# Kernel optimization log

Measured on AMD Instinct MI355X. Metric: run time of the kernel, lower is better.

Reference implementation:

```python
import jax, jax.numpy as jnp
import numpy as np

LN_EPS = 1e-5
NORM_EPS = 1e-6
ALPHA = 0.5

def _normalize_xyz_with_pc(pc, xyz):
    # center by point-cloud centroid, scale by max radius (per batch)
    c = pc.mean(axis=1, keepdims=True)                      # [B,1,3]
    scale = jnp.linalg.norm(pc - c, axis=-1).max(axis=1)    # [B]
    return (xyz - c) / (scale[:, None, None] + NORM_EPS)

def setup_inputs() -> dict:
    key = jax.random.key(0)
    ks = jax.random.split(key, 9)
    B, N, Ns, K, Dv, Dc = 4, 20000, 1024, 8192, 768, 256
    return {
        "point_cloud": jax.random.normal(ks[0], (B, N, 3), jnp.float32),
        "seed_xyz": jax.random.normal(ks[1], (B, Ns, 3), jnp.float32),
        "pts": jax.random.normal(ks[2], (B, K, 3), jnp.float32),
        "feat": jax.random.normal(ks[3], (B, Dv, K), jnp.float32),
        "f_graspnet": jax.random.normal(ks[4], (B, Dc, Ns), jnp.float32),
        "W_proj": jax.random.normal(ks[5], (Dc, Dv), jnp.float32) * 0.02,
        "b_proj": jnp.zeros((Dc,), jnp.float32),
        "W_a1": jax.random.normal(ks[6], (Dc, Dc), jnp.float32) * 0.05,
        "b_a1": jnp.zeros((Dc,), jnp.float32),
        "W_a2": jax.random.normal(ks[7], (Dc, Dc), jnp.float32) * 0.05,
        "b_a2": jnp.zeros((Dc,), jnp.float32),
    }

def reference(point_cloud, seed_xyz, pts, feat, f_graspnet,
              W_proj, b_proj, W_a1, b_a1, W_a2, b_a2):
    seed_n = _normalize_xyz_with_pc(point_cloud, seed_xyz)   # [B,Ns,3]
    pts_n = _normalize_xyz_with_pc(point_cloud, pts)         # [B,K,3]
    # squared pairwise distances [B,Ns,K] (argmin equivalent to cdist argmin)
    d2 = ((seed_n ** 2).sum(-1)[:, :, None]
          - 2.0 * jnp.einsum('bnd,bkd->bnk', seed_n, pts_n)
          + (pts_n ** 2).sum(-1)[:, None, :])
    idx = jnp.argmin(d2, axis=-1)                            # [B,Ns]
    vggt_raw = jnp.take_along_axis(feat, idx[:, None, :], axis=2)  # [B,768,Ns]
    # 1x1 conv projector 768->256
    x = jnp.einsum('oc,bcn->bon', W_proj, vggt_raw) + b_proj[None, :, None]
    # LayerNorm over channel dim, no affine
    mu = x.mean(axis=1, keepdims=True)
    var = ((x - mu) ** 2).mean(axis=1, keepdims=True)
    x_ln = (x - mu) / jnp.sqrt(var + LN_EPS)
    # adapter: conv-relu-conv (all 1x1)
    h = jax.nn.relu(jnp.einsum('oc,bcn->bon', W_a1, x_ln) + b_a1[None, :, None])
    f_adapt = jnp.einsum('oc,bcn->bon', W_a2, h) + b_a2[None, :, None]
    return (1.0 - ALPHA) * f_graspnet + ALPHA * f_adapt
```

## Files before the change

kernel.cpp:

```cpp
#include <hip/hip_runtime.h>
#include <hip/hip_bf16.h>
#include <math.h>

#define LN_EPS 1e-5f

constexpr int BB  = 4;
constexpr int NS  = 1024;
constexpr int KP  = 8192;
constexpr int DV  = 768;
constexpr int DC  = 256;

using bf16x8 = __attribute__((ext_vector_type(8))) short;
using f32x4  = __attribute__((ext_vector_type(4))) float;

static __device__ __forceinline__ unsigned short f2bf(float v) {
    __hip_bfloat16 h = __float2bfloat16(v);
    return *reinterpret_cast<unsigned short*>(&h);
}

__global__ __launch_bounds__(256) void argmin_prep_kernel(
    const float* __restrict__ seed_xyz, const float* __restrict__ pts,
    int* __restrict__ out_idx,
    const float* __restrict__ Wp, const float* __restrict__ W1,
    const float* __restrict__ W2,
    unsigned short* __restrict__ Wpb, unsigned short* __restrict__ W1b,
    unsigned short* __restrict__ W2b)
{
    const int t = threadIdx.x;
    if (blockIdx.x >= 512) {
        int e  = (blockIdx.x - 512) * 256 + t;
        int e4 = e << 2;
        const float* src; unsigned short* dst; int off;
        if (e4 < DC * DV)              { src = Wp; dst = Wpb; off = e4; }
        else if (e4 < DC * (DV + DC))  { src = W1; dst = W1b; off = e4 - DC * DV; }
        else                           { src = W2; dst = W2b; off = e4 - DC * (DV + DC); }
        float4 v = *(const float4*)(src + off);
        ushort4 o;
        o.x = f2bf(v.x); o.y = f2bf(v.y); o.z = f2bf(v.z); o.w = f2bf(v.w);
        *(ushort4*)(dst + off) = o;
        return;
    }

    __shared__ float shX[1024], shY[1024], shZ[1024];
    __shared__ double rb[4][8];
    __shared__ int    ri[4][8];

    const int bid  = blockIdx.x;
    const int b    = bid >> 7;
    const int tile = bid & 127;

    double n2sx[8], n2sy[8], n2sz[8];
    {
        const float* sp = seed_xyz + ((size_t)b * NS + tile * 8) * 3;
        #pragma unroll
        for (int ss = 0; ss < 8; ++ss) {
            n2sx[ss] = -2.0 * (double)sp[ss * 3 + 0];
            n2sy[ss] = -2.0 * (double)sp[ss * 3 + 1];
            n2sz[ss] = -2.0 * (double)sp[ss * 3 + 2];
        }
    }

    const float* pb = pts + (size_t)b * KP * 3;
    double best[8];
    int    bidx[8];
    #pragma unroll
    for (int ss = 0; ss < 8; ++ss) { best[ss] = 1e300; bidx[ss] = 0; }

    for (int kt = 0; kt < KP; kt += 1024) {
        #pragma unroll
        for (int q = 0; q < 4; ++q) {
            int i = t + q * 256;
            const float* pp = pb + (size_t)(kt + i) * 3;
            shX[i] = pp[0]; shY[i] = pp[1]; shZ[i] = pp[2];
        }
        __syncthreads();
        #pragma unroll 2
        for (int q = 0; q < 4; ++q) {
            int kl = t + (q << 8);
            double px = (double)shX[kl];
            double py = (double)shY[kl];
            double pz = (double)shZ[kl];
            double h  = fma(px, px, fma(py, py, pz * pz));
            #pragma unroll
            for (int ss = 0; ss < 8; ++ss) {
                double acc = fma(n2sx[ss], px, h);
                acc = fma(n2sy[ss], py, acc);
                acc = fma(n2sz[ss], pz, acc);
                if (acc < best[ss]) { best[ss] = acc; bidx[ss] = kt + kl; }
            }
        }
        __syncthreads();
    }

    #pragma unroll
    for (int o = 1; o < 64; o <<= 1) {
        #pragma unroll
        for (int ss = 0; ss < 8; ++ss) {
            double ob = __shfl_xor(best[ss], o);
            int    oi = __shfl_xor(bidx[ss], o);
            if (ob < best[ss] || (ob == best[ss] && oi < bidx[ss])) {
                best[ss] = ob; bidx[ss] = oi;
            }
        }
    }
    const int w = t >> 6, l = t & 63;
    if (l == 0) {
        #pragma unroll
        for (int ss = 0; ss < 8; ++ss) { rb[w][ss] = best[ss]; ri[w][ss] = bidx[ss]; }
    }
    __syncthreads();
    if (t < 8) {
        double bb = rb[0][t]; int bi = ri[0][t];
        #pragma unroll
        for (int ww = 1; ww < 4; ++ww) {
            double ob = rb[ww][t]; int oi = ri[ww][t];
            if (ob < bb || (ob == bb && oi < bi)) { bb = ob; bi = oi; }
        }
        out_idx[b * NS + tile * 8 + t] = bi;
    }
}

__global__ __launch_bounds__(512, 4) void proj_kernel(
    const float* __restrict__ feat, const int* __restrict__ idx,
    const unsigned short* __restrict__ Wpb, float* __restrict__ Xg)
{
    __shared__ unsigned short LDSB[64 * 40];
    __shared__ int ent_s[1024];
    __shared__ int ent_k[1024];
    __shared__ int nent;

    const int bid = blockIdx.x;
    const int b   = bid >> 7;
    const int kt  = bid & 127;
    const int k0  = kt * 64;
    const int t   = threadIdx.x;
    const int w   = t >> 6;
    const int l   = t & 63;
    const int col = l & 15;
    const int kq  = l >> 4;

    if (t == 0) nent = 0;
    __syncthreads();
    {
        int ka = idx[b * NS + t];
        int kb = idx[b * NS + 512 + t];
        if (ka >= k0 && ka < k0 + 64) { int p = atomicAdd(&nent, 1); ent_s[p] = t;       ent_k[p] = ka; }
        if (kb >= k0 && kb < k0 + 64) { int p = atomicAdd(&nent, 1); ent_s[p] = 512 + t; ent_k[p] = kb; }
    }

    const int cc = t >> 4;
    const int k4 = t & 15;
    const float* fbase = feat + ((size_t)b * DV + cc) * KP + k0 + k4 * 4;

    f32x4 acc0[4], acc1[4];
    #pragma unroll
    for (int kg = 0; kg < 4; ++kg) {
        acc0[kg] = (f32x4){0.f, 0.f, 0.f, 0.f};
        acc1[kg] = (f32x4){0.f, 0.f, 0.f, 0.f};
    }

    f32x4 r = *(const f32x4*)(fbase);
    for (int s = 0; s < 24; ++s) {
        if (s) __syncthreads();
        {
            const int kr0 = k4 * 4;
            const int cb  = cc >> 3;
            const int cl  = cc & 7;
            #pragma unroll
            for (int i = 0; i < 4; ++i) {
                int krow = kr0 + i;
                int qv   = ((krow >> 2) ^ (krow >> 4)) & 3;
                LDSB[krow * 40 + ((cb ^ qv) << 3) + cl] = f2bf(r[i]);
            }
        }
        if (s + 1 < 24)
            r = *(const f32x4*)(fbase + (size_t)(s + 1) * 32 * KP);
        __syncthreads();
        const unsigned short* A0 = Wpb + (size_t)(w * 32 + col) * DV + s * 32 + kq * 8;
        bf16x8 a0 = *(const bf16x8*)A0;
        bf16x8 a1 = *(const bf16x8*)(A0 + (size_t)16 * DV);
        #pragma unroll
        for (int kg = 0; kg < 4; ++kg) {
            int krow = kg * 16 + col;
            int qv   = ((krow >> 2) ^ (krow >> 4)) & 3;
            bf16x8 bf = *(const bf16x8*)&LDSB[krow * 40 + ((kq ^ qv) << 3)];
            acc0[kg] = __builtin_amdgcn_mfma_f32_16x16x32_bf16(a0, bf, acc0[kg], 0, 0, 0);
            acc1[kg] = __builtin_amdgcn_mfma_f32_16x16x32_bf16(a1, bf, acc1[kg], 0, 0, 0);
        }
    }
    __syncthreads();

    const int ne = nent;
    for (int e = 0; e < ne; ++e) {
        int sd = ent_s[e];
        int kk = ent_k[e] - k0;
        if (col == (kk & 15)) {
            int j = kk >> 4;
            float* dst = Xg + ((size_t)(b * NS + sd)) * DC + w * 32 + kq * 4;
            #pragma unroll
            for (int jj = 0; jj < 4; ++jj) if (jj == j) {
                *(f32x4*)dst        = acc0[jj];
                *(f32x4*)(dst + 16) = acc1[jj];
            }
        }
    }
}

__global__ __launch_bounds__(512) void mega_kernel(
    const float* __restrict__ Xg,
    const float* __restrict__ fg,
    const float* __restrict__ bp,
    const unsigned short* __restrict__ W1b, const float* __restrict__ b1,
    const unsigned short* __restrict__ W2b, const float* __restrict__ b2,
    float* __restrict__ out)
{
    __shared__ alignas(16) unsigned short XT[16][264];
    __shared__ alignas(16) unsigned short HT[16][264];
    __shared__ float LNs[8][16];
    __shared__ float LNq[8][16];

    const int bid  = blockIdx.x;
    const int b    = bid >> 6;
    const int tile = bid & 63;
    const int n0   = tile * 16;
    const int t    = threadIdx.x;
    const int w    = t >> 6;
    const int l    = t & 63;
    const int col  = l & 15;
    const int kq   = l >> 4;

    const float* fgb = fg + (size_t)b * DC * NS;
    float fgv[8];
    #pragma unroll
    for (int r = 0; r < 4; ++r) {
        int ch0 = w * 32 + kq * 4 + r;
        fgv[r]     = fgb[(size_t)ch0 * NS + n0 + col];
        fgv[4 + r] = fgb[(size_t)(ch0 + 16) * NS + n0 + col];
    }

    const float* xr = Xg + ((size_t)(b * NS + n0 + col)) * DC + w * 32 + kq * 4;
    f32x4 x0 = *(const f32x4*)xr;
    f32x4 x1 = *(const f32x4*)(xr + 16);

    float vals[8];
    float s = 0.f, q = 0.f;
    #pragma unroll
    for (int r = 0; r < 4; ++r) {
        int ch0 = w * 32 + kq * 4 + r;
        float v0 = x0[r] + bp[ch0];
        float v1 = x1[r] + bp[ch0 + 16];
        vals[r]     = v0;
        vals[4 + r] = v1;
        s += v0 + v1;
        q += v0 * v0 + v1 * v1;
    }
    s += __shfl_xor(s, 16); s += __shfl_xor(s, 32);
    q += __shfl_xor(q, 16); q += __shfl_xor(q, 32);
    if (l < 16) { LNs[w][l] = s; LNq[w][l] = q; }
    __syncthreads();
    float S = 0.f, Q = 0.f;
    #pragma unroll
    for (int ww = 0; ww < 8; ++ww) { S += LNs[ww][col]; Q += LNq[ww][col]; }
    float mu   = S * (1.0f / DC);
    float rstd = rsqrtf(Q * (1.0f / DC) - mu * mu + LN_EPS);
    {
        ushort4 p0, p1;
        p0.x = f2bf((vals[0] - mu) * rstd);
        p0.y = f2bf((vals[1] - mu) * rstd);
        p0.z = f2bf((vals[2] - mu) * rstd);
        p0.w = f2bf((vals[3] - mu) * rstd);
        p1.x = f2bf((vals[4] - mu) * rstd);
        p1.y = f2bf((vals[5] - mu) * rstd);
        p1.z = f2bf((vals[6] - mu) * rstd);
        p1.w = f2bf((vals[7] - mu) * rstd);
        *(ushort4*)&XT[col][w * 32 + kq * 4]      = p0;
        *(ushort4*)&XT[col][w * 32 + 16 + kq * 4] = p1;
    }
    __syncthreads();

    f32x4 acc0 = {0.f, 0.f, 0.f, 0.f};
    f32x4 acc1 = {0.f, 0.f, 0.f, 0.f};
    {
        const unsigned short* A0 = W1b + (size_t)(w * 32 + col) * DC;
        const unsigned short* A1 = W1b + (size_t)(w * 32 + 16 + col) * DC;
        #pragma unroll
        for (int ks = 0; ks < 8; ++ks) {
            int kb = ks * 32 + kq * 8;
            bf16x8 bf = *(const bf16x8*)&XT[col][kb];
            bf16x8 a0 = *(const bf16x8*)&A0[kb];
            bf16x8 a1 = *(const bf16x8*)&A1[kb];
            acc0 = __builtin_amdgcn_mfma_f32_16x16x32_bf16(a0, bf, acc0, 0, 0, 0);
            acc1 = __builtin_amdgcn_mfma_f32_16x16x32_bf16(a1, bf, acc1, 0, 0, 0);
        }
    }
    {
        ushort4 p0, p1;
        int ch0 = w * 32 + kq * 4;
        p0.x = f2bf(fmaxf(acc0[0] + b1[ch0 + 0], 0.f));
        p0.y = f2bf(fmaxf(acc0[1] + b1[ch0 + 1], 0.f));
        p0.z = f2bf(fmaxf(acc0[2] + b1[ch0 + 2], 0.f));
        p0.w = f2bf(fmaxf(acc0[3] + b1[ch0 + 3], 0.f));
        p1.x = f2bf(fmaxf(acc1[0] + b1[ch0 + 16], 0.f));
        p1.y = f2bf(fmaxf(acc1[1] + b1[ch0 + 17], 0.f));
        p1.z = f2bf(fmaxf(acc1[2] + b1[ch0 + 18], 0.f));
        p1.w = f2bf(fmaxf(acc1[3] + b1[ch0 + 19], 0.f));
        *(ushort4*)&HT[col][ch0]      = p0;
        *(ushort4*)&HT[col][ch0 + 16] = p1;
    }
    __syncthreads();

    acc0 = (f32x4){0.f, 0.f, 0.f, 0.f};
    acc1 = (f32x4){0.f, 0.f, 0.f, 0.f};
    {
        const unsigned short* A0 = W2b + (size_t)(w * 32 + col) * DC;
        const unsigned short* A1 = W2b + (size_t)(w * 32 + 16 + col) * DC;
        #pragma unroll
        for (int ks = 0; ks < 8; ++ks) {
            int kb = ks * 32 + kq * 8;
            bf16x8 bf = *(const bf16x8*)&HT[col][kb];
            bf16x8 a0 = *(const bf16x8*)&A0[kb];
            bf16x8 a1 = *(const bf16x8*)&A1[kb];
            acc0 = __builtin_amdgcn_mfma_f32_16x16x32_bf16(a0, bf, acc0, 0, 0, 0);
            acc1 = __builtin_amdgcn_mfma_f32_16x16x32_bf16(a1, bf, acc1, 0, 0, 0);
        }
    }
    {
        float* ob = out + (size_t)b * DC * NS;
        #pragma unroll
        for (int r = 0; r < 4; ++r) {
            int ch0 = w * 32 + kq * 4 + r;
            int ch1 = ch0 + 16;
            size_t o0 = (size_t)ch0 * NS + n0 + col;
            size_t o1 = (size_t)ch1 * NS + n0 + col;
            ob[o0] = 0.5f * fgv[r]     + 0.5f * (acc0[r] + b2[ch0]);
            ob[o1] = 0.5f * fgv[4 + r] + 0.5f * (acc1[r] + b2[ch1]);
        }
    }
}

extern "C" void kernel_launch(void* const* d_in, const int* in_sizes, int n_in,
                              void* d_out, int out_size, void* d_ws, size_t ws_size,
                              hipStream_t stream)
{
    (void)in_sizes; (void)n_in; (void)out_size; (void)ws_size;
    const float* seed_xyz = (const float*)d_in[1];
    const float* pts      = (const float*)d_in[2];
    const float* feat     = (const float*)d_in[3];
    const float* fgn      = (const float*)d_in[4];
    const float* Wp       = (const float*)d_in[5];
    const float* bp       = (const float*)d_in[6];
    const float* W1       = (const float*)d_in[7];
    const float* b1       = (const float*)d_in[8];
    const float* W2       = (const float*)d_in[9];
    const float* b2       = (const float*)d_in[10];
    float* out = (float*)d_out;

    char* ws = (char*)d_ws;
    int*            idx = (int*)ws;
    unsigned short* Wpb = (unsigned short*)(ws + 16384);
    unsigned short* W1b = (unsigned short*)(ws + 409600);
    unsigned short* W2b = (unsigned short*)(ws + 540672);
    float*          Xg  = (float*)(ws + 671744);

    argmin_prep_kernel<<<dim3(832), dim3(256), 0, stream>>>(
        seed_xyz, pts, idx, Wp, W1, W2, Wpb, W1b, W2b);
    proj_kernel<<<dim3(512), dim3(512), 0, stream>>>(feat, idx, Wpb, Xg);
    mega_kernel<<<dim3(BB * (NS / 16)), dim3(512), 0, stream>>>(
        Xg, fgn, bp, W1b, b1, W2b, b2, out);
}
```

Before: 66.76 us.

## Fuse projection with LN/adapter kernel, double-buffer LDS, pack argmin index into distance bits

Result: slower. 110.6 us (+65.6%).

```diff
diff --git a/kernel.cpp b/kernel.cpp
--- a/kernel.cpp
+++ b/kernel.cpp
@@ -43,7 +43,6 @@
 
     __shared__ float shX[1024], shY[1024], shZ[1024];
     __shared__ double rb[4][8];
-    __shared__ int    ri[4][8];
 
     const int bid  = blockIdx.x;
     const int b    = bid >> 7;
@@ -62,9 +61,8 @@
 
     const float* pb = pts + (size_t)b * KP * 3;
     double best[8];
-    int    bidx[8];
     #pragma unroll
-    for (int ss = 0; ss < 8; ++ss) { best[ss] = 1e300; bidx[ss] = 0; }
+    for (int ss = 0; ss < 8; ++ss) best[ss] = 1e300;
 
     for (int kt = 0; kt < KP; kt += 1024) {
         #pragma unroll
@@ -81,12 +79,15 @@
             double py = (double)shY[kl];
             double pz = (double)shZ[kl];
             double h  = fma(px, px, fma(py, py, pz * pz));
+            long long kidx = (long long)(kt + kl);
             #pragma unroll
             for (int ss = 0; ss < 8; ++ss) {
                 double acc = fma(n2sx[ss], px, h);
                 acc = fma(n2sy[ss], py, acc);
                 acc = fma(n2sz[ss], pz, acc);
-                if (acc < best[ss]) { best[ss] = acc; bidx[ss] = kt + kl; }
+                long long bits = __double_as_longlong(acc);
+                bits = (bits & 0xFFFFFFFFFFFFE000LL) | kidx;
+                best[ss] = fmin(best[ss], __longlong_as_double(bits));
             }
         }
         __syncthreads();
@@ -95,39 +96,41 @@
     #pragma unroll
     for (int o = 1; o < 64; o <<= 1) {
         #pragma unroll
-        for (int ss = 0; ss < 8; ++ss) {
-            double ob = __shfl_xor(best[ss], o);
-            int    oi = __shfl_xor(bidx[ss], o);
-            if (ob < best[ss] || (ob == best[ss] && oi < bidx[ss])) {
-                best[ss] = ob; bidx[ss] = oi;
-            }
-        }
+        for (int ss = 0; ss < 8; ++ss)
+            best[ss] = fmin(best[ss], __shfl_xor(best[ss], o));
     }
     const int w = t >> 6, l = t & 63;
     if (l == 0) {
         #pragma unroll
-        for (int ss = 0; ss < 8; ++ss) { rb[w][ss] = best[ss]; ri[w][ss] = bidx[ss]; }
+        for (int ss = 0; ss < 8; ++ss) rb[w][ss] = best[ss];
     }
     __syncthreads();
     if (t < 8) {
-        double bb = rb[0][t]; int bi = ri[0][t];
-        #pragma unroll
-        for (int ww = 1; ww < 4; ++ww) {
-            double ob = rb[ww][t]; int oi = ri[ww][t];
-            if (ob < bb || (ob == bb && oi < bi)) { bb = ob; bi = oi; }
-        }
-        out_idx[b * NS + tile * 8 + t] = bi;
+        double bb = rb[0][t];
+        #pragma unroll
+        for (int ww = 1; ww < 4; ++ww) bb = fmin(bb, rb[ww][t]);
+        out_idx[b * NS + tile * 8 + t] =
+            (int)(__double_as_longlong(bb) & 0x1FFFLL);
     }
 }
 
-__global__ __launch_bounds__(512, 4) void proj_kernel(
+__global__ __launch_bounds__(512, 4) void projmega_kernel(
     const float* __restrict__ feat, const int* __restrict__ idx,
-    const unsigned short* __restrict__ Wpb, float* __restrict__ Xg)
+    const unsigned short* __restrict__ Wpb, const float* __restrict__ bp,
+    const unsigned short* __restrict__ W1b, const float* __restrict__ b1,
+    const unsigned short* __restrict__ W2b, const float* __restrict__ b2,
+    const float* __restrict__ fg, float* __restrict__ out)
 {
-    __shared__ unsigned short LDSB[64 * 40];
+    __shared__ alignas(16) char ubuf[16 * 260 * 4];
+    unsigned short* LDSB = (unsigned short*)ubuf;
+    float*          XF   = (float*)ubuf;
     __shared__ int ent_s[1024];
     __shared__ int ent_k[1024];
     __shared__ int nent;
+    __shared__ alignas(16) unsigned short XT[16][264];
+    __shared__ alignas(16) unsigned short HT[16][264];
+    __shared__ float LNs[8][16];
+    __shared__ float LNq[8][16];
 
     const int bid = blockIdx.x;
     const int b   = bid >> 7;
@@ -160,180 +163,190 @@
     }
 
     f32x4 r = *(const f32x4*)(fbase);
+    {
+        const int kr0 = k4 * 4, cb = cc >> 3, cl = cc & 7;
+        #pragma unroll
+        for (int i = 0; i < 4; ++i) {
+            int krow = kr0 + i;
+            int qv   = ((krow >> 2) ^ (krow >> 4)) & 3;
+            LDSB[krow * 40 + ((cb ^ qv) << 3) + cl] = f2bf(r[i]);
+        }
+    }
+    r = *(const f32x4*)(fbase + (size_t)32 * KP);
+    __syncthreads();
+
+    const float* fgb = fg + (size_t)b * DC * NS;
+    float fgp[8];
+    const int neE = nent;
+    if (neE > 0) {
+        int sd0 = ent_s[(col < neE) ? col : 0];
+        #pragma unroll
+        for (int rr = 0; rr < 4; ++rr) {
+            int ch0 = w * 32 + kq * 4 + rr;
+            fgp[rr]     = fgb[(size_t)ch0 * NS + sd0];
+            fgp[4 + rr] = fgb[(size_t)(ch0 + 16) * NS + sd0];
+        }
+    }
+
     for (int s = 0; s < 24; ++s) {
-        if (s) __syncthreads();
-        {
-            const int kr0 = k4 * 4;
-            const int cb  = cc >> 3;
-            const int cl  = cc & 7;
+        if (s + 1 < 24) {
+            const int kr0 = k4 * 4, cb = cc >> 3, cl = cc & 7;
+            unsigned short* Lb = LDSB + ((s + 1) & 1) * (64 * 40);
             #pragma unroll
             for (int i = 0; i < 4; ++i) {
                 int krow = kr0 + i;
                 int qv   = ((krow >> 2) ^ (krow >> 4)) & 3;
-                LDSB[krow * 40 + ((cb ^ qv) << 3) + cl] = f2bf(r[i]);
-            }
-        }
-        if (s + 1 < 24)
-            r = *(const f32x4*)(fbase + (size_t)(s + 1) * 32 * KP);
-        __syncthreads();
+                Lb[krow * 40 + ((cb ^ qv) << 3) + cl] = f2bf(r[i]);
+            }
+        }
+        if (s + 2 < 24)
+            r = *(const f32x4*)(fbase + (size_t)(s + 2) * 32 * KP);
+
         const unsigned short* A0 = Wpb + (size_t)(w * 32 + col) * DV + s * 32 + kq * 8;
         bf16x8 a0 = *(const bf16x8*)A0;
         bf16x8 a1 = *(const bf16x8*)(A0 + (size_t)16 * DV);
+        const unsigned short* Lr = LDSB + (s & 1) * (64 * 40);
         #pragma unroll
         for (int kg = 0; kg < 4; ++kg) {
             int krow = kg * 16 + col;
             int qv   = ((krow >> 2) ^ (krow >> 4)) & 3;
-            bf16x8 bf = *(const bf16x8*)&LDSB[krow * 40 + ((kq ^ qv) << 3)];
+            bf16x8 bf = *(const bf16x8*)&Lr[krow * 40 + ((kq ^ qv) << 3)];
             acc0[kg] = __builtin_amdgcn_mfma_f32_16x16x32_bf16(a0, bf, acc0[kg], 0, 0, 0);
             acc1[kg] = __builtin_amdgcn_mfma_f32_16x16x32_bf16(a1, bf, acc1[kg], 0, 0, 0);
         }
-    }
-    __syncthreads();
-
-    const int ne = nent;
-    for (int e = 0; e < ne; ++e) {
-        int sd = ent_s[e];
-        int kk = ent_k[e] - k0;
-        if (col == (kk & 15)) {
-            int j = kk >> 4;
-            float* dst = Xg + ((size_t)(b * NS + sd)) * DC + w * 32 + kq * 4;
-            #pragma unroll
-            for (int jj = 0; jj < 4; ++jj) if (jj == j) {
-                *(f32x4*)dst        = acc0[jj];
-                *(f32x4*)(dst + 16) = acc1[jj];
-            }
-        }
-    }
-}
-
-__global__ __launch_bounds__(512) void mega_kernel(
-    const float* __restrict__ Xg,
-    const float* __restrict__ fg,
-    const float* __restrict__ bp,
-    const unsigned short* __restrict__ W1b, const float* __restrict__ b1,
-    const unsigned short* __restrict__ W2b, const float* __restrict__ b2,
-    float* __restrict__ out)
-{
-    __shared__ alignas(16) unsigned short XT[16][264];
-    __shared__ alignas(16) unsigned short HT[16][264];
-    __shared__ float LNs[8][16];
-    __shared__ float LNq[8][16];
-
-    const int bid  = blockIdx.x;
-    const int b    = bid >> 6;
-    const int tile = bid & 63;
-    const int n0   = tile * 16;
-    const int t    = threadIdx.x;
-    const int w    = t >> 6;
-    const int l    = t & 63;
-    const int col  = l & 15;
-    const int kq   = l >> 4;
-
-    const float* fgb = fg + (size_t)b * DC * NS;
-    float fgv[8];
-    #pragma unroll
-    for (int r = 0; r < 4; ++r) {
-        int ch0 = w * 32 + kq * 4 + r;
-        fgv[r]     = fgb[(size_t)ch0 * NS + n0 + col];
-        fgv[4 + r] = fgb[(size_t)(ch0 + 16) * NS + n0 + col];
-    }
-
-    const float* xr = Xg + ((size_t)(b * NS + n0 + col)) * DC + w * 32 + kq * 4;
-    f32x4 x0 = *(const f32x4*)xr;
-    f32x4 x1 = *(const f32x4*)(xr + 16);
-
-    float vals[8];
-    float s = 0.f, q = 0.f;
-    #pragma unroll
-    for (int r = 0; r < 4; ++r) {
-        int ch0 = w * 32 + kq * 4 + r;
-        float v0 = x0[r] + bp[ch0];
-        float v1 = x1[r] + bp[ch0 + 16];
-        vals[r]     = v0;
-        vals[4 + r] = v1;
-        s += v0 + v1;
-        q += v0 * v0 + v1 * v1;
-    }
-    s += __shfl_xor(s, 16); s += __shfl_xor(s, 32);
-    q += __shfl_xor(q, 16); q += __shfl_xor(q, 32);
-    if (l < 16) { LNs[w][l] = s; LNq[w][l] = q; }
-    __syncthreads();
-    float S = 0.f, Q = 0.f;
-    #pragma unroll
-    for (int ww = 0; ww < 8; ++ww) { S += LNs[ww][col]; Q += LNq[ww][col]; }
-    float mu   = S * (1.0f / DC);
-    float rstd = rsqrtf(Q * (1.0f / DC) - mu * mu + LN_EPS);
-    {
-        ushort4 p0, p1;
-        p0.x = f2bf((vals[0] - mu) * rstd);
-        p0.y = f2bf((vals[1] - mu) * rstd);
-        p0.z = f2bf((vals[2] - mu) * rstd);
-        p0.w = f2bf((vals[3] - mu) * rstd);
-        p1.x = f2bf((vals[4] - mu) * rstd);
-        p1.y = f2bf((vals[5] - mu) * rstd);
-        p1.z = f2bf((vals[6] - mu) * rstd);
-        p1.w = f2bf((vals[7] - mu) * rstd);
-        *(ushort4*)&XT[col][w * 32 + kq * 4]      = p0;
-        *(ushort4*)&XT[col][w * 32 + 16 + kq * 4] = p1;
-    }
-    __syncthreads();
-
-    f32x4 acc0 = {0.f, 0.f, 0.f, 0.f};
-    f32x4 acc1 = {0.f, 0.f, 0.f, 0.f};
-    {
-        const unsigned short* A0 = W1b + (size_t)(w * 32 + col) * DC;
-        const unsigned short* A1 = W1b + (size_t)(w * 32 + 16 + col) * DC;
-        #pragma unroll
-        for (int ks = 0; ks < 8; ++ks) {
-            int kb = ks * 32 + kq * 8;
-            bf16x8 bf = *(const bf16x8*)&XT[col][kb];
-            bf16x8 a0 = *(const bf16x8*)&A0[kb];
-            bf16x8 a1 = *(const bf16x8*)&A1[kb];
-            acc0 = __builtin_amdgcn_mfma_f32_16x16x32_bf16(a0, bf, acc0, 0, 0, 0);
-            acc1 = __builtin_amdgcn_mfma_f32_16x16x32_bf16(a1, bf, acc1, 0, 0, 0);
-        }
-    }
-    {
-        ushort4 p0, p1;
-        int ch0 = w * 32 + kq * 4;
-        p0.x = f2bf(fmaxf(acc0[0] + b1[ch0 + 0], 0.f));
-        p0.y = f2bf(fmaxf(acc0[1] + b1[ch0 + 1], 0.f));
-        p0.z = f2bf(fmaxf(acc0[2] + b1[ch0 + 2], 0.f));
-        p0.w = f2bf(fmaxf(acc0[3] + b1[ch0 + 3], 0.f));
-        p1.x = f2bf(fmaxf(acc1[0] + b1[ch0 + 16], 0.f));
-        p1.y = f2bf(fmaxf(acc1[1] + b1[ch0 + 17], 0.f));
-        p1.z = f2bf(fmaxf(acc1[2] + b1[ch0 + 18], 0.f));
-        p1.w = f2bf(fmaxf(acc1[3] + b1[ch0 + 19], 0.f));
-        *(ushort4*)&HT[col][ch0]      = p0;
-        *(ushort4*)&HT[col][ch0 + 16] = p1;
-    }
-    __syncthreads();
-
-    acc0 = (f32x4){0.f, 0.f, 0.f, 0.f};
-    acc1 = (f32x4){0.f, 0.f, 0.f, 0.f};
-    {
-        const unsigned short* A0 = W2b + (size_t)(w * 32 + col) * DC;
-        const unsigned short* A1 = W2b + (size_t)(w * 32 + 16 + col) * DC;
-        #pragma unroll
-        for (int ks = 0; ks < 8; ++ks) {
-            int kb = ks * 32 + kq * 8;
-            bf16x8 bf = *(const bf16x8*)&HT[col][kb];
-            bf16x8 a0 = *(const bf16x8*)&A0[kb];
-            bf16x8 a1 = *(const bf16x8*)&A1[kb];
-            acc0 = __builtin_amdgcn_mfma_f32_16x16x32_bf16(a0, bf, acc0, 0, 0, 0);
-            acc1 = __builtin_amdgcn_mfma_f32_16x16x32_bf16(a1, bf, acc1, 0, 0, 0);
-        }
-    }
-    {
-        float* ob = out + (size_t)b * DC * NS;
-        #pragma unroll
-        for (int r = 0; r < 4; ++r) {
-            int ch0 = w * 32 + kq * 4 + r;
-            int ch1 = ch0 + 16;
-            size_t o0 = (size_t)ch0 * NS + n0 + col;
-            size_t o1 = (size_t)ch1 * NS + n0 + col;
-            ob[o0] = 0.5f * fgv[r]     + 0.5f * (acc0[r] + b2[ch0]);
-            ob[o1] = 0.5f * fgv[4 + r] + 0.5f * (acc1[r] + b2[ch1]);
+        __syncthreads();
+    }
+
+    const int ne = neE;
+    for (int e0 = 0; e0 < ne; e0 += 16) {
+        __syncthreads();
+        const int nc = (ne - e0 < 16) ? (ne - e0) : 16;
+
+        for (int e = e0; e < e0 + nc; ++e) {
+            int kk = ent_k[e] - k0;
+            if (col == (kk & 15)) {
+                int j = kk >> 4;
+                float* dst = XF + (e - e0) * 260 + w * 32 + kq * 4;
+                #pragma unroll
+                for (int jj = 0; jj < 4; ++jj) if (jj == j) {
+                    *(f32x4*)dst        = acc0[jj];
+                    *(f32x4*)(dst + 16) = acc1[jj];
+                }
+            }
+        }
+        __syncthreads();
+
+        const bool valid = (col < nc);
+        const int  sd    = ent_s[e0 + (valid ? col : 0)];
+
+        float fgv[8];
+        if (e0 == 0) {
+            #pragma unroll
+            for (int rr = 0; rr < 8; ++rr) fgv[rr] = fgp[rr];
+        } else {
+            #pragma unroll
+            for (int rr = 0; rr < 4; ++rr) {
+                int ch0 = w * 32 + kq * 4 + rr;
+                fgv[rr]     = fgb[(size_t)ch0 * NS + sd];
+                fgv[4 + rr] = fgb[(size_t)(ch0 + 16) * NS + sd];
+            }
+        }
+
+        const float* xr = XF + col * 260 + w * 32 + kq * 4;
+        f32x4 x0 = *(const f32x4*)xr;
+        f32x4 x1 = *(const f32x4*)(xr + 16);
+
+        float vals[8];
+        float s = 0.f, q = 0.f;
+        #pragma unroll
+        for (int rr = 0; rr < 4; ++rr) {
+            int ch0 = w * 32 + kq * 4 + rr;
+            float v0 = x0[rr] + bp[ch0];
+            float v1 = x1[rr] + bp[ch0 + 16];
+            vals[rr]     = v0;
+            vals[4 + rr] = v1;
+            s += v0 + v1;
+            q += v0 * v0 + v1 * v1;
+        }
+        s += __shfl_xor(s, 16); s += __shfl_xor(s, 32);
+        q += __shfl_xor(q, 16); q += __shfl_xor(q, 32);
+        if (l < 16) { LNs[w][l] = s; LNq[w][l] = q; }
+        __syncthreads();
+        float S = 0.f, Q = 0.f;
+        #pragma unroll
+        for (int ww = 0; ww < 8; ++ww) { S += LNs[ww][col]; Q += LNq[ww][col]; }
+        float mu   = S * (1.0f / DC);
+        float rstd = rsqrtf(Q * (1.0f / DC) - mu * mu + LN_EPS);
+        {
+            ushort4 p0, p1;
+            p0.x = f2bf((vals[0] - mu) * rstd);
+            p0.y = f2bf((vals[1] - mu) * rstd);
+            p0.z = f2bf((vals[2] - mu) * rstd);
+            p0.w = f2bf((vals[3] - mu) * rstd);
+            p1.x = f2bf((vals[4] - mu) * rstd);
+            p1.y = f2bf((vals[5] - mu) * rstd);
+            p1.z = f2bf((vals[6] - mu) * rstd);
+            p1.w = f2bf((vals[7] - mu) * rstd);
+            *(ushort4*)&XT[col][w * 32 + kq * 4]      = p0;
+            *(ushort4*)&XT[col][w * 32 + 16 + kq * 4] = p1;
+        }
+        __syncthreads();
+
+        f32x4 c0 = {0.f, 0.f, 0.f, 0.f};
+        f32x4 c1 = {0.f, 0.f, 0.f, 0.f};
+        {
+            const unsigned short* A0 = W1b + (size_t)(w * 32 + col) * DC;
+            const unsigned short* A1 = W1b + (size_t)(w * 32 + 16 + col) * DC;
+            #pragma unroll
+            for (int ks = 0; ks < 8; ++ks) {
+                int kb = ks * 32 + kq * 8;
+                bf16x8 bf = *(const bf16x8*)&XT[col][kb];
+                bf16x8 a0 = *(const bf16x8*)&A0[kb];
+                bf16x8 a1 = *(const bf16x8*)&A1[kb];
+                c0 = __builtin_amdgcn_mfma_f32_16x16x32_bf16(a0, bf, c0, 0, 0, 0);
+                c1 = __builtin_amdgcn_mfma_f32_16x16x32_bf16(a1, bf, c1, 0, 0, 0);
+            }
+        }
+        {
+            ushort4 p0, p1;
+            int ch0 = w * 32 + kq * 4;
+            p0.x = f2bf(fmaxf(c0[0] + b1[ch0 + 0], 0.f));
+            p0.y = f2bf(fmaxf(c0[1] + b1[ch0 + 1], 0.f));
+            p0.z = f2bf(fmaxf(c0[2] + b1[ch0 + 2], 0.f));
+            p0.w = f2bf(fmaxf(c0[3] + b1[ch0 + 3], 0.f));
+            p1.x = f2bf(fmaxf(c1[0] + b1[ch0 + 16], 0.f));
+            p1.y = f2bf(fmaxf(c1[1] + b1[ch0 + 17], 0.f));
+            p1.z = f2bf(fmaxf(c1[2] + b1[ch0 + 18], 0.f));
+            p1.w = f2bf(fmaxf(c1[3] + b1[ch0 + 19], 0.f));
+            *(ushort4*)&HT[col][ch0]      = p0;
+            *(ushort4*)&HT[col][ch0 + 16] = p1;
+        }
+        __syncthreads();
+
+        c0 = (f32x4){0.f, 0.f, 0.f, 0.f};
+        c1 = (f32x4){0.f, 0.f, 0.f, 0.f};
+        {
+            const unsigned short* A0 = W2b + (size_t)(w * 32 + col) * DC;
+            const unsigned short* A1 = W2b + (size_t)(w * 32 + 16 + col) * DC;
+            #pragma unroll
+            for (int ks = 0; ks < 8; ++ks) {
+                int kb = ks * 32 + kq * 8;
+                bf16x8 bf = *(const bf16x8*)&HT[col][kb];
+                bf16x8 a0 = *(const bf16x8*)&A0[kb];
+                bf16x8 a1 = *(const bf16x8*)&A1[kb];
+                c0 = __builtin_amdgcn_mfma_f32_16x16x32_bf16(a0, bf, c0, 0, 0, 0);
+                c1 = __builtin_amdgcn_mfma_f32_16x16x32_bf16(a1, bf, c1, 0, 0, 0);
+            }
+        }
+        if (valid) {
+            float* ob = out + (size_t)b * DC * NS;
+            #pragma unroll
+            for (int rr = 0; rr < 4; ++rr) {
+                int ch0 = w * 32 + kq * 4 + rr;
+                int ch1 = ch0 + 16;
+                ob[(size_t)ch0 * NS + sd] = 0.5f * fgv[rr]     + 0.5f * (c0[rr] + b2[ch0]);
+                ob[(size_t)ch1 * NS + sd] = 0.5f * fgv[4 + rr] + 0.5f * (c1[rr] + b2[ch1]);
+            }
         }
     }
 }
@@ -360,11 +373,9 @@
     unsigned short* Wpb = (unsigned short*)(ws + 16384);
     unsigned short* W1b = (unsigned short*)(ws + 409600);
     unsigned short* W2b = (unsigned short*)(ws + 540672);
-    float*          Xg  = (float*)(ws + 671744);
 
     argmin_prep_kernel<<<dim3(832), dim3(256), 0, stream>>>(
         seed_xyz, pts, idx, Wp, W1, W2, Wpb, W1b, W2b);
-    proj_kernel<<<dim3(512), dim3(512), 0, stream>>>(feat, idx, Wpb, Xg);
-    mega_kernel<<<dim3(BB * (NS / 16)), dim3(512), 0, stream>>>(
-        Xg, fgn, bp, W1b, b1, W2b, b2, out);
+    projmega_kernel<<<dim3(512), dim3(512), 0, stream>>>(
+        feat, idx, Wpb, bp, W1b, b1, W2b, b2, fgn, out);
 }
```
